# Optimization experiments

Hardware: AMD Instinct MI355X
Metric: run time of the kernel (lower is better)

## Reference

```python
import jax, jax.numpy as jnp
import numpy as np

MULTI_INFER_NUM = 8
D_EMBED = 128
T, B = 512, 32


def setup_inputs() -> dict:
    key = jax.random.key(0)
    k1, k2, k3 = jax.random.split(key, 3)
    positions = jax.random.randint(k1, (T, B), 0, 16, dtype=jnp.int64)
    outputs = jax.random.normal(k2, (T, B, D_EMBED), dtype=jnp.float32)
    table = jax.random.normal(k3, (MULTI_INFER_NUM + 1, D_EMBED, D_EMBED), dtype=jnp.float32)
    return {"positions": positions, "outputs": outputs, "table": table}


def reference(positions, outputs, table):
    # clip positions >= multi_infer_num to the sentinel row multi_infer_num
    r_positions = jnp.where(positions < MULTI_INFER_NUM, positions, MULTI_INFER_NUM)
    # gather per-(t,b) d x d transfer matrices: [T, B, d, d]
    positions_embedding = table[r_positions]
    # batched matvec: [T, B, d]
    transferred = jnp.einsum('ibde,ibd->ibe', positions_embedding, outputs)
    return transferred
```

## Files before the change

kernel.cpp:

```cpp
#include <hip/hip_runtime.h>

#define DEMB    128
#define LSTRIDE 130

using short8 = __attribute__((ext_vector_type(8))) short;
using f32x4  = __attribute__((ext_vector_type(4))) float;

__device__ __forceinline__ unsigned short f2bf(float f) {
    unsigned u = __float_as_uint(f);
    u = u + 0x7FFFu + ((u >> 16) & 1u);
    return (unsigned short)(u >> 16);
}
__device__ __forceinline__ unsigned pack2(float a, float b) {
    return (unsigned)f2bf(a) | ((unsigned)f2bf(b) << 16);
}

__global__ __launch_bounds__(256) void mpt_kernel(
    const int*   __restrict__ positions,
    const float* __restrict__ table,
    const float* __restrict__ x,
    float*       __restrict__ out) {

    __shared__ unsigned short sm[128 * LSTRIDE];
    __shared__ uint4 frag[2048];
    __shared__ int   sel[512];
    __shared__ int   scnt;

    const int bid = blockIdx.x;
    const int tid = threadIdx.x;

    int r, base, npos;
    if (bid < 256) { r = 8; base = bid * 64;  npos = 64;  }
    else { r = (bid - 256) >> 5; base = ((bid - 256) & 31) * 512; npos = 512; }

    if (tid == 0) scnt = 0;
    __syncthreads();

    const float* Mr = table + r * DEMB * DEMB;
    float4 st[16];
#pragma unroll
    for (int f4 = 0; f4 < 16; ++f4) {
        const int id  = f4 * 256 + tid;
        const int row = id >> 5;
        const int c4  = id & 31;
        st[f4] = ((const float4*)(Mr + row * DEMB))[c4];
    }

    for (int i = tid; i < npos; i += 256) {
        const int p = positions[base + i];
        const bool hit = (r == 8) ? (p >= 8) : (p == r);
        if (hit) { const int k = atomicAdd(&scnt, 1); sel[k] = base + i; }
    }

#pragma unroll
    for (int f4 = 0; f4 < 16; ++f4) {
        const int id  = f4 * 256 + tid;
        const int row = id >> 5;
        const int c4  = id & 31;
        unsigned* dst = (unsigned*)&sm[row * LSTRIDE + c4 * 4];
        dst[0] = pack2(st[f4].x, st[f4].y);
        dst[1] = pack2(st[f4].z, st[f4].w);
    }
    __syncthreads();

#pragma unroll
    for (int f = 0; f < 8; ++f) {
        const int fid  = f * 256 + tid;
        const int lane = fid & 63;
        const int ks   = (fid >> 6) & 3;
        const int nt   = fid >> 8;
        const int e    = nt * 16 + (lane & 15);
        const int d0   = ks * 32 + ((lane >> 4) << 3);
        union { unsigned short us[8]; uint4 v; } u;
#pragma unroll
        for (int j = 0; j < 8; ++j)
            u.us[j] = sm[(d0 + j) * LSTRIDE + e];
        frag[fid] = u.v;
    }
    __syncthreads();

    const int wave = tid >> 6;
    const int lane = tid & 63;
    const int m16  = lane & 15;
    const int quad = lane >> 4;
    const int cnt  = scnt;

    for (int tb = wave * 16; tb < cnt; tb += 64) {
        const int nm = ((cnt - tb) < 16) ? (cnt - tb) : 16;

        const int slotA = sel[tb + ((m16 < nm) ? m16 : 0)];
        const float* xrow = x + (size_t)slotA * DEMB;
        short8 a[4];
#pragma unroll
        for (int ks = 0; ks < 4; ++ks) {
            const float4* s4 = (const float4*)(xrow + ks * 32 + quad * 8);
            const float4 f0 = s4[0];
            const float4 f1 = s4[1];
            union { unsigned short us[8]; short8 s8; } ua;
            ua.us[0] = f2bf(f0.x); ua.us[1] = f2bf(f0.y);
            ua.us[2] = f2bf(f0.z); ua.us[3] = f2bf(f0.w);
            ua.us[4] = f2bf(f1.x); ua.us[5] = f2bf(f1.y);
            ua.us[6] = f2bf(f1.z); ua.us[7] = f2bf(f1.w);
            a[ks] = ua.s8;
        }

        int  prow[4];
        bool pval[4];
#pragma unroll
        for (int i = 0; i < 4; ++i) {
            const int m = quad * 4 + i;
            pval[i] = m < nm;
            prow[i] = sel[tb + (pval[i] ? m : 0)];
        }

#pragma unroll 2
        for (int nt = 0; nt < 8; ++nt) {
            f32x4 acc = {0.f, 0.f, 0.f, 0.f};
#pragma unroll
            for (int ks = 0; ks < 4; ++ks) {
                union { uint4 v4; short8 s8; } ub;
                ub.v4 = frag[(nt * 4 + ks) * 64 + lane];
                acc = __builtin_amdgcn_mfma_f32_16x16x32_bf16(a[ks], ub.s8, acc, 0, 0, 0);
            }
            const int col = nt * 16 + m16;
#pragma unroll
            for (int i = 0; i < 4; ++i)
                if (pval[i])
                    out[(size_t)prow[i] * DEMB + col] = acc[i];
        }
    }
}

extern "C" void kernel_launch(void* const* d_in, const int* in_sizes, int n_in,
                              void* d_out, int out_size, void* d_ws, size_t ws_size,
                              hipStream_t stream) {
    const int*   positions = (const int*)d_in[0];
    const float* outputs   = (const float*)d_in[1];
    const float* table     = (const float*)d_in[2];
    float* out = (float*)d_out;

    hipLaunchKernelGGL(mpt_kernel, dim3(512), dim3(256), 0, stream,
                       positions, table, outputs, out);
}
```

Before: 70.42 us.

## Split row tiles into half-column work units and prefetch activations before frag build

Each 16-row tile is now split into two work units covering four column tiles each, so waves share work more evenly when a block has few selected rows. The first unit's activation rows and output indices are loaded before the shared-memory fragment transposition, so global load latency overlaps with that phase. The cost is that each activation row is loaded and converted twice (once per half), plus extra live registers for the prefetched floats.

```diff
diff --git a/kernel.cpp b/kernel.cpp
--- a/kernel.cpp
+++ b/kernel.cpp
@@ -63,14 +63,44 @@
     }
     __syncthreads();
 
+    const int wave = tid >> 6;
+    const int lane = tid & 63;
+    const int m16  = lane & 15;
+    const int quad = lane >> 4;
+    const int cnt  = scnt;
+    const int nu   = (((cnt + 15) >> 4) << 1);
+
+    float4 xf[8];
+    int  prow[4];
+    bool pval[4];
+    bool have = (wave < nu);
+    if (have) {
+        const int tb = (wave >> 1) * 16;
+        const int nm = ((cnt - tb) < 16) ? (cnt - tb) : 16;
+        const int slotA = sel[tb + ((m16 < nm) ? m16 : 0)];
+        const float* xrow = x + (size_t)slotA * DEMB;
+#pragma unroll
+        for (int ks = 0; ks < 4; ++ks) {
+            const float4* s4 = (const float4*)(xrow + ks * 32 + quad * 8);
+            xf[2 * ks]     = s4[0];
+            xf[2 * ks + 1] = s4[1];
+        }
+#pragma unroll
+        for (int i = 0; i < 4; ++i) {
+            const int m = quad * 4 + i;
+            pval[i] = m < nm;
+            prow[i] = sel[tb + (pval[i] ? m : 0)];
+        }
+    }
+
 #pragma unroll
     for (int f = 0; f < 8; ++f) {
         const int fid  = f * 256 + tid;
-        const int lane = fid & 63;
+        const int ln   = fid & 63;
         const int ks   = (fid >> 6) & 3;
         const int nt   = fid >> 8;
-        const int e    = nt * 16 + (lane & 15);
-        const int d0   = ks * 32 + ((lane >> 4) << 3);
+        const int e    = nt * 16 + (ln & 15);
+        const int d0   = ks * 32 + ((ln >> 4) << 3);
         union { unsigned short us[8]; uint4 v; } u;
 #pragma unroll
         for (int j = 0; j < 8; ++j)
@@ -79,23 +109,34 @@
     }
     __syncthreads();
 
-    const int wave = tid >> 6;
-    const int lane = tid & 63;
-    const int m16  = lane & 15;
-    const int quad = lane >> 4;
-    const int cnt  = scnt;
+    for (int u = wave; u < nu; u += 4) {
+        const int tb  = (u >> 1) * 16;
+        const int nt0 = (u & 1) << 2;
+        const int nm  = ((cnt - tb) < 16) ? (cnt - tb) : 16;
 
-    for (int tb = wave * 16; tb < cnt; tb += 64) {
-        const int nm = ((cnt - tb) < 16) ? (cnt - tb) : 16;
+        if (!have) {
+            const int slotA = sel[tb + ((m16 < nm) ? m16 : 0)];
+            const float* xrow = x + (size_t)slotA * DEMB;
+#pragma unroll
+            for (int ks = 0; ks < 4; ++ks) {
+                const float4* s4 = (const float4*)(xrow + ks * 32 + quad * 8);
+                xf[2 * ks]     = s4[0];
+                xf[2 * ks + 1] = s4[1];
+            }
+#pragma unroll
+            for (int i = 0; i < 4; ++i) {
+                const int m = quad * 4 + i;
+                pval[i] = m < nm;
+                prow[i] = sel[tb + (pval[i] ? m : 0)];
+            }
+        }
+        have = false;
 
-        const int slotA = sel[tb + ((m16 < nm) ? m16 : 0)];
-        const float* xrow = x + (size_t)slotA * DEMB;
         short8 a[4];
 #pragma unroll
         for (int ks = 0; ks < 4; ++ks) {
-            const float4* s4 = (const float4*)(xrow + ks * 32 + quad * 8);
-            const float4 f0 = s4[0];
-            const float4 f1 = s4[1];
+            const float4 f0 = xf[2 * ks];
+            const float4 f1 = xf[2 * ks + 1];
             union { unsigned short us[8]; short8 s8; } ua;
             ua.us[0] = f2bf(f0.x); ua.us[1] = f2bf(f0.y);
             ua.us[2] = f2bf(f0.z); ua.us[3] = f2bf(f0.w);
@@ -104,25 +145,17 @@
             a[ks] = ua.s8;
         }
 
-        int  prow[4];
-        bool pval[4];
 #pragma unroll
-        for (int i = 0; i < 4; ++i) {
-            const int m = quad * 4 + i;
-            pval[i] = m < nm;
-            prow[i] = sel[tb + (pval[i] ? m : 0)];
-        }
-
-#pragma unroll 2
-        for (int nt = 0; nt < 8; ++nt) {
+        for (int nt = 0; nt < 4; ++nt) {
+            const int ntt = nt0 + nt;
             f32x4 acc = {0.f, 0.f, 0.f, 0.f};
 #pragma unroll
             for (int ks = 0; ks < 4; ++ks) {
                 union { uint4 v4; short8 s8; } ub;
-                ub.v4 = frag[(nt * 4 + ks) * 64 + lane];
+                ub.v4 = frag[(ntt * 4 + ks) * 64 + lane];
                 acc = __builtin_amdgcn_mfma_f32_16x16x32_bf16(a[ks], ub.s8, acc, 0, 0, 0);
             }
-            const int col = nt * 16 + m16;
+            const int col = ntt * 16 + m16;
 #pragma unroll
             for (int i = 0; i < 4; ++i)
                 if (pval[i])
```

New measurement: 71.31 us. No clear change (+1.3%).
